# Kernel optimization log

Hardware: AMD Instinct MI355X
Metric: run time of the kernel (lower is better)

The kernel has to match this reference:

```python
import jax, jax.numpy as jnp
import numpy as np

NUM_CLASSES = 80
INP_DIM = 608
NUM_ANCHORS = 3


def setup_inputs() -> dict:
    key = jax.random.key(0)
    B, G = 16, 76
    C = NUM_ANCHORS * (NUM_CLASSES + 5)  # 255
    prediction = jax.random.normal(key, (B, C, G, G), dtype=jnp.float32)
    anchors = jnp.array([[116.0, 90.0], [156.0, 198.0], [373.0, 326.0]], dtype=jnp.float32)
    return {"prediction": prediction, "anchors": anchors}


def reference(prediction, anchors):
    B = prediction.shape[0]
    G = prediction.shape[2]
    A = anchors.shape[0]
    NC = NUM_CLASSES
    stride = INP_DIM / G  # python float, static

    # [B, A, NC+5, G, G] -> [B, A, G, G, NC+5]
    p = prediction.reshape(B, A, NC + 5, G, G).transpose(0, 1, 3, 4, 2)

    scaled_anchors = anchors / jnp.float32(stride)          # [A, 2]
    anchor_w = scaled_anchors[:, 0].reshape(1, A, 1, 1)
    anchor_h = scaled_anchors[:, 1].reshape(1, A, 1, 1)

    x = jax.nn.sigmoid(p[..., 0])
    y = jax.nn.sigmoid(p[..., 1])
    w = p[..., 2]
    h = p[..., 3]
    pred_conf = jax.nn.sigmoid(p[..., 4])
    pred_cls = jax.nn.sigmoid(p[..., 5:])

    grid = jnp.arange(G, dtype=p.dtype)
    x_offset = grid.reshape(1, 1, 1, G)   # varies along last (column) axis
    y_offset = grid.reshape(1, 1, G, 1)   # varies along row axis

    bx = x + x_offset
    by = y + y_offset
    bw = jnp.exp(w) * anchor_w
    bh = jnp.exp(h) * anchor_h
    pred_boxes = jnp.stack([bx, by, bw, bh], axis=-1)  # [B, A, G, G, 4]

    output = jnp.concatenate(
        [
            pred_boxes.reshape(B, -1, 4) * jnp.float32(stride),
            pred_conf.reshape(B, -1, 1),
            pred_cls.reshape(B, -1, NC),
        ],
        axis=-1,
    )  # [B, A*G*G, NC+5]
    return output
```

## Files before the change

### kernel.cpp

```cpp
#include <hip/hip_runtime.h>


#define GDIM 76
#define GG 5776
#define NA 3
#define NCH 85
#define TILE 128
#define THREADS 512
#define LOAD_UNITS (NCH * (TILE / 4))
#define LITERS 6
#define TPB 46
#define NT (TPB * NA * 16)
#define GRID 768

__device__ __forceinline__ float fast_sigmoid(float x) {
    return __builtin_amdgcn_rcpf(1.0f + __expf(-x));
}

__global__ __launch_bounds__(THREADS) void yolo_kernel(
    const float* __restrict__ in, const float* __restrict__ anchors,
    float* __restrict__ out)
{
    __shared__ float lds[TILE * NCH];

    const int t = threadIdx.x;

    float4 v[LITERS];

    auto load_tile = [&](int g) {
        int ba   = g / TPB;
        int tile = g - ba * TPB;
        int s0   = tile * TILE;
        const float* inb = in + (long)ba * (NCH * GG);
        #pragma unroll
        for (int i = 0; i < LITERS; ++i) {
            int idx = t + i * THREADS;
            int c   = idx >> 5;
            int q   = idx & 31;
            int pos = s0 + q * 4;
            if (idx < LOAD_UNITS && pos < GG)
                v[i] = *reinterpret_cast<const float4*>(&inb[(long)c * GG + pos]);
        }
    };

    auto transform_write = [&](int g) {
        int ba   = g / TPB;
        int tile = g - ba * TPB;
        int a    = ba % NA;
        int s0   = tile * TILE;
        float aw = anchors[2 * a];
        float ah = anchors[2 * a + 1];
        #pragma unroll
        for (int i = 0; i < LITERS; ++i) {
            int idx = t + i * THREADS;
            int c   = idx >> 5;
            int q   = idx & 31;
            int pos = s0 + q * 4;
            if (idx < LOAD_UNITS && pos < GG) {
                float r[4] = {v[i].x, v[i].y, v[i].z, v[i].w};
                if (c == 0) {
                    #pragma unroll
                    for (int k = 0; k < 4; ++k) {
                        int p = pos + k;
                        float gx = (float)(p - (p / GDIM) * GDIM);
                        r[k] = (fast_sigmoid(r[k]) + gx) * 8.0f;
                    }
                } else if (c == 1) {
                    #pragma unroll
                    for (int k = 0; k < 4; ++k) {
                        int p = pos + k;
                        float gy = (float)(p / GDIM);
                        r[k] = (fast_sigmoid(r[k]) + gy) * 8.0f;
                    }
                } else if (c == 2) {
                    #pragma unroll
                    for (int k = 0; k < 4; ++k) r[k] = __expf(r[k]) * aw;
                } else if (c == 3) {
                    #pragma unroll
                    for (int k = 0; k < 4; ++k) r[k] = __expf(r[k]) * ah;
                } else {
                    #pragma unroll
                    for (int k = 0; k < 4; ++k) r[k] = fast_sigmoid(r[k]);
                }
                #pragma unroll
                for (int k = 0; k < 4; ++k)
                    lds[(q * 4 + k) * NCH + c] = r[k];
            }
        }
    };

    auto store_tile = [&](int g) {
        int ba    = g / TPB;
        int tile  = g - ba * TPB;
        int s0    = tile * TILE;
        int valid = (GG - s0 < TILE) ? (GG - s0) : TILE;
        int n4    = valid * NCH / 4;
        float4* __restrict__ outv =
            reinterpret_cast<float4*>(out + ((long)ba * GG + s0) * NCH);
        const float4* ldsv = reinterpret_cast<const float4*>(lds);
        #pragma unroll
        for (int i = 0; i < LITERS; ++i) {
            int f4 = t + i * THREADS;
            if (f4 < n4)
                outv[f4] = ldsv[f4];
        }
    };

    int g = blockIdx.x;
    load_tile(g);
    for (; g < NT; g += GRID) {
        transform_write(g);
        __syncthreads();
        int gn = g + GRID;
        if (gn < NT) load_tile(gn);
        store_tile(g);
        __syncthreads();
    }
}

extern "C" void kernel_launch(void* const* d_in, const int* in_sizes, int n_in,
                              void* d_out, int out_size, void* d_ws, size_t ws_size,
                              hipStream_t stream) {
    const float* pred    = (const float*)d_in[0];
    const float* anchors = (const float*)d_in[1];
    float* out           = (float*)d_out;

    yolo_kernel<<<dim3(GRID), dim3(THREADS), 0, stream>>>(pred, anchors, out);
}
```

Before: 33.76 us.

## Replace persistent tile loop with one-shot blocks loading a 256-position pair

```diff
diff --git a/kernel.cpp b/kernel.cpp
--- a/kernel.cpp
+++ b/kernel.cpp
@@ -5,13 +5,14 @@
 #define GG 5776
 #define NA 3
 #define NCH 85
-#define TILE 128
+#define PAIR 256
+#define HALF 128
 #define THREADS 512
-#define LOAD_UNITS (NCH * (TILE / 4))
-#define LITERS 6
-#define TPB 46
-#define NT (TPB * NA * 16)
-#define GRID 768
+#define PPB 23
+#define NBLK (PPB * NA * 16)
+#define UNITS (NCH * (PAIR / 4))
+#define LITERS 11
+#define SITERS 6
 
 __device__ __forceinline__ float fast_sigmoid(float x) {
     return __builtin_amdgcn_rcpf(1.0f + __expf(-x));
@@ -21,101 +22,98 @@
     const float* __restrict__ in, const float* __restrict__ anchors,
     float* __restrict__ out)
 {
-    __shared__ float lds[TILE * NCH];
+    __shared__ float lds[HALF * NCH];
 
-    const int t = threadIdx.x;
+    const int t  = threadIdx.x;
+    const int bp = blockIdx.x;
+    const int ba = bp / PPB;
+    const int p  = bp - ba * PPB;
+    const int a  = ba % NA;
+    const int s0 = p * PAIR;
+
+    const float aw = anchors[2 * a];
+    const float ah = anchors[2 * a + 1];
+    const float* inb = in + (long)ba * (NCH * GG);
 
     float4 v[LITERS];
 
-    auto load_tile = [&](int g) {
-        int ba   = g / TPB;
-        int tile = g - ba * TPB;
-        int s0   = tile * TILE;
-        const float* inb = in + (long)ba * (NCH * GG);
+    #pragma unroll
+    for (int i = 0; i < LITERS; ++i) {
+        int u = t + i * THREADS;
+        if (u < UNITS) {
+            int c = u >> 6, q = u & 63;
+            int pos = s0 + q * 4;
+            if (pos < GG)
+                v[i] = *reinterpret_cast<const float4*>(&inb[(long)c * GG + pos]);
+        }
+    }
+
+    auto transform_half = [&](int h) {
         #pragma unroll
         for (int i = 0; i < LITERS; ++i) {
-            int idx = t + i * THREADS;
-            int c   = idx >> 5;
-            int q   = idx & 31;
-            int pos = s0 + q * 4;
-            if (idx < LOAD_UNITS && pos < GG)
-                v[i] = *reinterpret_cast<const float4*>(&inb[(long)c * GG + pos]);
-        }
-    };
-
-    auto transform_write = [&](int g) {
-        int ba   = g / TPB;
-        int tile = g - ba * TPB;
-        int a    = ba % NA;
-        int s0   = tile * TILE;
-        float aw = anchors[2 * a];
-        float ah = anchors[2 * a + 1];
-        #pragma unroll
-        for (int i = 0; i < LITERS; ++i) {
-            int idx = t + i * THREADS;
-            int c   = idx >> 5;
-            int q   = idx & 31;
-            int pos = s0 + q * 4;
-            if (idx < LOAD_UNITS && pos < GG) {
-                float r[4] = {v[i].x, v[i].y, v[i].z, v[i].w};
-                if (c == 0) {
-                    #pragma unroll
-                    for (int k = 0; k < 4; ++k) {
-                        int p = pos + k;
-                        float gx = (float)(p - (p / GDIM) * GDIM);
-                        r[k] = (fast_sigmoid(r[k]) + gx) * 8.0f;
+            int u = t + i * THREADS;
+            if (u < UNITS) {
+                int c = u >> 6, q = u & 63;
+                if ((q >> 5) == h) {
+                    int pos = s0 + q * 4;
+                    if (pos < GG) {
+                        int qr = q & 31;
+                        float r[4] = {v[i].x, v[i].y, v[i].z, v[i].w};
+                        if (c == 0) {
+                            #pragma unroll
+                            for (int k = 0; k < 4; ++k) {
+                                int pp = pos + k;
+                                float gx = (float)(pp - (pp / GDIM) * GDIM);
+                                r[k] = (fast_sigmoid(r[k]) + gx) * 8.0f;
+                            }
+                        } else if (c == 1) {
+                            #pragma unroll
+                            for (int k = 0; k < 4; ++k) {
+                                int pp = pos + k;
+                                float gy = (float)(pp / GDIM);
+                                r[k] = (fast_sigmoid(r[k]) + gy) * 8.0f;
+                            }
+                        } else if (c == 2) {
+                            #pragma unroll
+                            for (int k = 0; k < 4; ++k) r[k] = __expf(r[k]) * aw;
+                        } else if (c == 3) {
+                            #pragma unroll
+                            for (int k = 0; k < 4; ++k) r[k] = __expf(r[k]) * ah;
+                        } else {
+                            #pragma unroll
+                            for (int k = 0; k < 4; ++k) r[k] = fast_sigmoid(r[k]);
+                        }
+                        #pragma unroll
+                        for (int k = 0; k < 4; ++k)
+                            lds[(qr * 4 + k) * NCH + c] = r[k];
                     }
-                } else if (c == 1) {
-                    #pragma unroll
-                    for (int k = 0; k < 4; ++k) {
-                        int p = pos + k;
-                        float gy = (float)(p / GDIM);
-                        r[k] = (fast_sigmoid(r[k]) + gy) * 8.0f;
-                    }
-                } else if (c == 2) {
-                    #pragma unroll
-                    for (int k = 0; k < 4; ++k) r[k] = __expf(r[k]) * aw;
-                } else if (c == 3) {
-                    #pragma unroll
-                    for (int k = 0; k < 4; ++k) r[k] = __expf(r[k]) * ah;
-                } else {
-                    #pragma unroll
-                    for (int k = 0; k < 4; ++k) r[k] = fast_sigmoid(r[k]);
                 }
-                #pragma unroll
-                for (int k = 0; k < 4; ++k)
-                    lds[(q * 4 + k) * NCH + c] = r[k];
             }
         }
     };
 
-    auto store_tile = [&](int g) {
-        int ba    = g / TPB;
-        int tile  = g - ba * TPB;
-        int s0    = tile * TILE;
-        int valid = (GG - s0 < TILE) ? (GG - s0) : TILE;
+    auto store_half = [&](int h) {
+        int hs0   = s0 + h * HALF;
+        int valid = (GG - hs0 < HALF) ? (GG - hs0) : HALF;
         int n4    = valid * NCH / 4;
         float4* __restrict__ outv =
-            reinterpret_cast<float4*>(out + ((long)ba * GG + s0) * NCH);
+            reinterpret_cast<float4*>(out + ((long)ba * GG + hs0) * NCH);
         const float4* ldsv = reinterpret_cast<const float4*>(lds);
         #pragma unroll
-        for (int i = 0; i < LITERS; ++i) {
+        for (int i = 0; i < SITERS; ++i) {
             int f4 = t + i * THREADS;
             if (f4 < n4)
                 outv[f4] = ldsv[f4];
         }
     };
 
-    int g = blockIdx.x;
-    load_tile(g);
-    for (; g < NT; g += GRID) {
-        transform_write(g);
-        __syncthreads();
-        int gn = g + GRID;
-        if (gn < NT) load_tile(gn);
-        store_tile(g);
-        __syncthreads();
-    }
+    transform_half(0);
+    __syncthreads();
+    store_half(0);
+    __syncthreads();
+    transform_half(1);
+    __syncthreads();
+    store_half(1);
 }
 
 extern "C" void kernel_launch(void* const* d_in, const int* in_sizes, int n_in,
@@ -125,5 +123,5 @@
     const float* anchors = (const float*)d_in[1];
     float* out           = (float*)d_out;
 
-    yolo_kernel<<<dim3(GRID), dim3(THREADS), 0, stream>>>(pred, anchors, out);
+    yolo_kernel<<<dim3(NBLK), dim3(THREADS), 0, stream>>>(pred, anchors, out);
 }
```

After: 38.55 us. 1.14x slower.
